# Performance work log

Hardware: AMD Instinct MI355X
Metric: run time of the kernel (lower is better)

The kernel has to match this reference:

```python
import jax, jax.numpy as jnp
import numpy as np

EPS = 1e-5
N_IN, N_OUT = 100000, 400000
C_IN, C = 64, 32
K = 27
M_UP, M_C = 100000, 120000


def _sparse_conv(x, w, in_idx, out_idx, n_out):
    # gather-matmul-scatter over K kernel-offset maps
    g = x[in_idx]                               # [K, M, Cin]
    c = jnp.einsum('kmc,kcd->kmd', g, w)        # [K, M, Cout]
    return jax.ops.segment_sum(c.reshape(-1, c.shape[-1]),
                               out_idx.reshape(-1).astype(jnp.int32),
                               num_segments=n_out)


def _bn(x, gamma, beta):
    # train-mode batch norm over the voxel dimension
    m = jnp.mean(x, axis=0)
    v = jnp.var(x, axis=0)
    return (x - m) * jax.lax.rsqrt(v + EPS) * gamma + beta


def setup_inputs() -> dict:
    key = jax.random.key(0)
    ks = jax.random.split(key, 12)
    inp = {
        'x': jax.random.normal(ks[0], (N_IN, C_IN), jnp.float32),
        'x_skip': jax.random.normal(ks[1], (N_OUT, C), jnp.float32),
        'w_up': jax.random.normal(ks[2], (K, C_IN, C), jnp.float32) * 0.05,
        'b_up': jnp.zeros((C,), jnp.float32),
        'g_up': jnp.ones((C,), jnp.float32),
        'bt_up': jnp.zeros((C,), jnp.float32),
        'w1': jax.random.normal(ks[3], (K, 2 * C, C), jnp.float32) * 0.05,
        'g1': jnp.ones((C,), jnp.float32),
        'bt1': jnp.zeros((C,), jnp.float32),
        'w2': jax.random.normal(ks[4], (K, C, C), jnp.float32) * 0.05,
        'g2': jnp.ones((C,), jnp.float32),
        'bt2': jnp.zeros((C,), jnp.float32),
        'up_in_idx': jax.random.randint(ks[5], (K, M_UP), 0, N_IN, jnp.int32),
        'up_out_idx': jax.random.randint(ks[6], (K, M_UP), 0, N_OUT, jnp.int32),
        'c1_in_idx': jax.random.randint(ks[7], (K, M_C), 0, N_OUT, jnp.int32),
        'c1_out_idx': jax.random.randint(ks[8], (K, M_C), 0, N_OUT, jnp.int32),
        'c2_in_idx': jax.random.randint(ks[9], (K, M_C), 0, N_OUT, jnp.int32),
        'c2_out_idx': jax.random.randint(ks[10], (K, M_C), 0, N_OUT, jnp.int32),
    }
    return inp


def reference(x, x_skip, w_up, b_up, g_up, bt_up, w1, g1, bt1, w2, g2, bt2,
              up_in_idx, up_out_idx, c1_in_idx, c1_out_idx, c2_in_idx, c2_out_idx):
    n_out = x_skip.shape[0]
    # transposed sparse upconv onto the skip grid (+ bias)
    h = _sparse_conv(x, w_up, up_in_idx, up_out_idx, n_out) + b_up
    h = jax.nn.relu(_bn(h, g_up, bt_up))
    # jcat along channel dim
    h = jnp.concatenate([h, x_skip], axis=1)      # [N_out, 2C]
    # conv1 (3x3x3, bias=False) + BN + ReLU
    h = _sparse_conv(h, w1, c1_in_idx, c1_out_idx, n_out)
    h = jax.nn.relu(_bn(h, g1, bt1))
    # conv2 (3x3x3, bias=False) + BN + ReLU
    h = _sparse_conv(h, w2, c2_in_idx, c2_out_idx, n_out)
    h = jax.nn.relu(_bn(h, g2, bt2))
    return h
```

## Files before the change

kernel.cpp:

```cpp
#include <hip/hip_runtime.h>

#define EPS_BN 1e-5f

typedef unsigned int u32;
typedef short short8 __attribute__((ext_vector_type(8)));
typedef float f32x16 __attribute__((ext_vector_type(16)));
typedef _Float16 h4 __attribute__((ext_vector_type(4)));
typedef _Float16 h8f __attribute__((ext_vector_type(8)));

constexpr int N_IN_C  = 100000;
constexpr int N_OUT_C = 400000;
constexpr int KTAPS   = 27;
constexpr int M_UP_C  = 100000;
constexpr int M_C_C   = 120000;

constexpr int WIN     = 256;
constexpr int SH      = 8;
constexpr int NWIN    = (N_OUT_C + WIN - 1) / WIN;
constexpr int NWIN_U  = (N_IN_C  + WIN - 1) / WIN;
constexpr int NBA     = NWIN * KTAPS;
constexpr int NBT     = 3 * NBA;
constexpr int SCHUNK  = 2048;
constexpr int FCH     = 8192;
constexpr int NCHK    = 15;
constexpr int MAXW    = 1600;
constexpr int WSLOTS  = 7;
constexpr int NTILES  = N_OUT_C / 128;
constexpr int HSZ     = 3 * KTAPS * NCHK * NWIN;
constexpr int ENTT    = 27 * (M_UP_C + 2 * M_C_C) + NBT * 31 + 64;

__device__ inline unsigned short f2bf(float f) {
    u32 u = __builtin_bit_cast(u32, f);
    return (unsigned short)((u + 0x7FFFu + ((u >> 16) & 1u)) >> 16);
}

__global__ __launch_bounds__(256) void cvt_kernel(
    const float* __restrict__ s, ushort* __restrict__ d, int n4)
{
    const int i = blockIdx.x * 256 + threadIdx.x;
    if (i >= n4) return;
    const float4 v = reinterpret_cast<const float4*>(s)[i];
    ushort4 o;
    o.x = f2bf(v.x); o.y = f2bf(v.y); o.z = f2bf(v.z); o.w = f2bf(v.w);
    reinterpret_cast<ushort4*>(d)[i] = o;
}

__global__ __launch_bounds__(256) void wpack_kernel(
    const float* __restrict__ wU, const float* __restrict__ w1,
    const float* __restrict__ w2,
    ushort* __restrict__ fU, ushort* __restrict__ f1, ushort* __restrict__ f2)
{
    const int t = blockIdx.x * 256 + threadIdx.x;
    const float* w; ushort* dst; int CIN, NF, local;
    if      (t <  6912) { w = wU; dst = fU; CIN = 64; NF = 4; local = t; }
    else if (t < 13824) { w = w1; dst = f1; CIN = 64; NF = 4; local = t - 6912; }
    else if (t < 17280) { w = w2; dst = f2; CIN = 32; NF = 2; local = t - 13824; }
    else return;
    const int lane = local & 63;
    const int fi   = (local >> 6) % NF;
    const int tap  = local / (64 * NF);
    const int half = lane >> 5, colc = lane & 31;
    ushort* o = dst + ((size_t)(tap * NF + fi) * 64 + lane) * 8;
#pragma unroll
    for (int j = 0; j < 8; ++j) {
        const int k = 16 * fi + 8 * half + j;
        o[j] = f2bf(w[((size_t)tap * CIN + k) * 32 + colc]);
    }
}

__global__ __launch_bounds__(256) void histx_kernel(
    const int* __restrict__ i0, const int* __restrict__ i1,
    const int* __restrict__ i2, u32* __restrict__ h)
{
    const int s = blockIdx.z, k = blockIdx.y, c = blockIdx.x;
    const int M    = (s == 0) ? M_UP_C : M_C_C;
    const int nwin = (s == 0) ? NWIN_U : NWIN;
    const int m0 = c * FCH;
    if (m0 >= M) return;
    const int cnt = min(FCH, M - m0);
    const int* idx = (s == 0) ? i0 : (s == 1) ? i1 : i2;

    __shared__ u32 lh[NWIN];
    for (int w = threadIdx.x; w < nwin; w += 256) lh[w] = 0;
    __syncthreads();
    const int* ink = idx + (size_t)k * M + m0;
    for (int i = threadIdx.x; i < cnt; i += 256)
        atomicAdd(&lh[ink[i] >> SH], 1u);
    __syncthreads();
    u32* hp = h + ((size_t)(s * KTAPS + k) * NCHK + c) * NWIN;
    for (int w = threadIdx.x; w < nwin; w += 256) hp[w] = lh[w];
}

__global__ __launch_bounds__(256) void totals_kernel(
    const u32* __restrict__ h, u32* __restrict__ cnt)
{
    const int s = blockIdx.z, k = blockIdx.y;
    const int w = blockIdx.x * 256 + threadIdx.x;
    if (w >= NWIN) return;
    const u32* hp = h + (size_t)(s * KTAPS + k) * NCHK * NWIN + w;
    u32 t = 0;
#pragma unroll
    for (int c = 0; c < NCHK; ++c) t += hp[(size_t)c * NWIN];
    cnt[(size_t)s * NBA + w * KTAPS + k] = t;
}

__global__ __launch_bounds__(256) void scan_part_kernel(
    const u32* __restrict__ cnt, u32* __restrict__ bsum, int nb)
{
    const int i0 = blockIdx.x * SCHUNK + threadIdx.x * 8;
    u32 s = 0;
#pragma unroll
    for (int j = 0; j < 8; ++j) {
        const int i = i0 + j;
        if (i < nb) s += (cnt[i] + 31u) & ~31u;
    }
    __shared__ u32 ls[256];
    ls[threadIdx.x] = s;
    __syncthreads();
    for (int off = 128; off > 0; off >>= 1) {
        if (threadIdx.x < off) ls[threadIdx.x] += ls[threadIdx.x + off];
        __syncthreads();
    }
    if (threadIdx.x == 0) bsum[blockIdx.x] = ls[0];
}

__global__ __launch_bounds__(1024) void scan_bsum_kernel(
    u32* __restrict__ bsum, int nblk)
{
    __shared__ u32 tmp[1024];
    const int t = threadIdx.x;
    const u32 v = (t < nblk) ? bsum[t] : 0u;
    tmp[t] = v;
    __syncthreads();
    for (int off = 1; off < 1024; off <<= 1) {
        const u32 u = (t >= off) ? tmp[t - off] : 0u;
        __syncthreads();
        tmp[t] += u;
        __syncthreads();
    }
    if (t < nblk) bsum[t] = tmp[t] - v;
}

__global__ __launch_bounds__(256) void scan_emit_kernel(
    const u32* __restrict__ cnt, const u32* __restrict__ bsum,
    u32* __restrict__ starts, int nb)
{
    const int t  = threadIdx.x;
    const int i0 = blockIdx.x * SCHUNK + t * 8;
    u32 vals[8];
    u32 s = 0;
#pragma unroll
    for (int j = 0; j < 8; ++j) {
        const int i = i0 + j;
        u32 c = (i < nb) ? cnt[i] : 0u;
        c = (c + 31u) & ~31u;
        vals[j] = c;
        s += c;
    }
    __shared__ u32 ls[256];
    ls[t] = s;
    __syncthreads();
    for (int off = 1; off < 256; off <<= 1) {
        const u32 u = (t >= off) ? ls[t - off] : 0u;
        __syncthreads();
        ls[t] += u;
        __syncthreads();
    }
    u32 run = bsum[blockIdx.x] + ls[t] - s;
#pragma unroll
    for (int j = 0; j < 8; ++j) {
        const int i = i0 + j;
        if (i < nb) starts[i] = run;
        run += vals[j];
    }
    if (blockIdx.x == gridDim.x - 1 && t == 255) starts[nb] = run;
}

__global__ __launch_bounds__(256) void pbase_kernel(
    const u32* __restrict__ h, const u32* __restrict__ starts,
    u32* __restrict__ pb)
{
    const int s = blockIdx.z, k = blockIdx.y;
    const int w = blockIdx.x * 256 + threadIdx.x;
    if (w >= NWIN) return;
    u32 run = starts[(size_t)s * NBA + w * KTAPS + k];
    const size_t base = (size_t)(s * KTAPS + k) * NCHK * NWIN + w;
#pragma unroll
    for (int c = 0; c < NCHK; ++c) {
        pb[base + (size_t)c * NWIN] = run;
        run += h[base + (size_t)c * NWIN];
    }
}

__global__ __launch_bounds__(256) void fill_kernel(
    const int* __restrict__ in0, const int* __restrict__ out0,
    const int* __restrict__ in1, const int* __restrict__ out1,
    const int* __restrict__ in2, const int* __restrict__ out2,
    const u32* __restrict__ pb, u32* __restrict__ entryA)
{
    __shared__ u32 hist[MAXW];
    __shared__ u32 lofs[MAXW];
    __shared__ u32 gbase[MAXW];
    __shared__ u32 lent[FCH];
    __shared__ u32 psum[256];

    const int s = blockIdx.z;
    const int* in_idx  = (s == 0) ? in0  : (s == 1) ? in1  : in2;
    const int* out_idx = (s == 0) ? out0 : (s == 1) ? out1 : out2;
    const int  M       = (s == 0) ? M_UP_C : M_C_C;
    const int  nwin    = (s == 0) ? NWIN_U : NWIN;

    const int k   = blockIdx.y;
    const int m0  = blockIdx.x * FCH;
    if (m0 >= M) return;
    const int cnt = min(FCH, M - m0);
    const int t   = threadIdx.x;

    const u32* pbk = pb + ((size_t)(s * KTAPS + k) * NCHK + blockIdx.x) * NWIN;

    for (int w = t; w < nwin; w += 256) {
        hist[w]  = 0;
        gbase[w] = pbk[w];
    }
    __syncthreads();

    const int* ink  = in_idx  + (size_t)k * M + m0;
    const int* outk = out_idx + (size_t)k * M + m0;

    for (int i = t; i < cnt; i += 256)
        atomicAdd(&hist[ink[i] >> SH], 1u);
    __syncthreads();

    u32 loc[WSLOTS];
    u32 ssum = 0;
#pragma unroll
    for (int j = 0; j < WSLOTS; ++j) {
        const int w = t * WSLOTS + j;
        const u32 c = (w < nwin) ? hist[w] : 0u;
        loc[j] = ssum;
        ssum += c;
    }
    psum[t] = ssum;
    __syncthreads();
    for (int off = 1; off < 256; off <<= 1) {
        const u32 v = (t >= off) ? psum[t - off] : 0u;
        __syncthreads();
        psum[t] += v;
        __syncthreads();
    }
    const u32 tbase = psum[t] - ssum;
#pragma unroll
    for (int j = 0; j < WSLOTS; ++j) {
        const int w = t * WSLOTS + j;
        if (w < nwin) lofs[w] = tbase + loc[j];
    }
    __syncthreads();

    for (int i = t; i < cnt; i += 256) {
        const int in = ink[i];
        const int o  = outk[i];
        const int w  = in >> SH;
        const u32 pp = atomicAdd(&lofs[w], 1u);
        lent[pp] = ((u32)(in & (WIN - 1)) << 19) | (u32)o;
    }
    __syncthreads();

    for (int w = t; w < nwin; w += 256) {
        const u32 c = hist[w];
        if (!c) continue;
        const u32 lo = lofs[w] - c;
        const u32 gb = gbase[w];
        for (u32 j = 0; j < c; ++j)
            entryA[gb + j] = lent[lo + j];
    }
}

template <int NF, int MODE>
__global__ __launch_bounds__(256) void conv_kernel(
    const void* __restrict__ srcAv, const void* __restrict__ srcBv,
    const ushort* __restrict__ wfrag,
    const u32* __restrict__ entryA, const u32* __restrict__ starts,
    const float* __restrict__ st, const float* __restrict__ g,
    const float* __restrict__ bt, float invn,
    _Float16* __restrict__ accH, int n_src)
{
    constexpr int NCH = NF * 2;
    constexpr int RPL = 8 / NCH;
    __shared__ ushort win[WIN * NF * 16];

    const int w0   = blockIdx.x * WIN;
    const int tid  = threadIdx.x;
    const int lane = tid & 63;
    const int wid  = tid >> 6;
    const int col  = lane & 31;
    const int half = lane >> 5;
    const int ch0  = tid % NCH;

    float sc8[8], bi8[8];
    const bool needbn = (MODE == 2) || (MODE == 1 && ch0 < 4);
    if (MODE != 0 && needbn) {
#pragma unroll
        for (int j = 0; j < 8; ++j) {
            const int c = ch0 * 8 + j;
            const float m   = st[c] * invn;
            const float var = fmaxf(st[32 + c] * invn - m * m, 0.f);
            const float s_  = rsqrtf(var + EPS_BN) * g[c];
            sc8[j] = s_;
            bi8[j] = fmaf(-m, s_, bt[c]);
        }
    }

    for (int i = tid; i < WIN * NCH; i += 256) {
        const int r  = i / NCH;
        const int row = w0 + r;
        short8 v = {0, 0, 0, 0, 0, 0, 0, 0};
        if (row < n_src) {
            if (MODE == 0) {
                const float* sp = (const float*)srcAv + (size_t)row * 64 + ch0 * 8;
#pragma unroll
                for (int j = 0; j < 8; ++j) v[j] = (short)f2bf(sp[j]);
            } else if (MODE == 1) {
                if (ch0 < 4) {
                    const h8f hv = *reinterpret_cast<const h8f*>(
                        (const _Float16*)srcAv + (size_t)row * 32 + ch0 * 8);
#pragma unroll
                    for (int j = 0; j < 8; ++j) {
                        const float y = fmaf(sc8[j], (float)hv[j], bi8[j]);
                        v[j] = (short)f2bf(y > 0.f ? y : 0.f);
                    }
                } else {
                    v = *reinterpret_cast<const short8*>(
                        (const ushort*)srcBv + (size_t)row * 32 + (ch0 - 4) * 8);
                }
            } else {
                const h8f hv = *reinterpret_cast<const h8f*>(
                    (const _Float16*)srcAv + (size_t)row * 32 + ch0 * 8);
#pragma unroll
                for (int j = 0; j < 8; ++j) {
                    const float y = fmaf(sc8[j], (float)hv[j], bi8[j]);
                    v[j] = (short)f2bf(y > 0.f ? y : 0.f);
                }
            }
        }
        const int addr = (r / RPL) * 64 + ((((r % RPL) * NCH + ch0) ^ ((r / RPL) & 7)) * 8);
        *reinterpret_cast<short8*>(&win[addr]) = v;
    }
    __syncthreads();

    const short8* wf8 = reinterpret_cast<const short8*>(wfrag);

    for (int tap = blockIdx.y * 4 + wid; tap < KTAPS; tap += 8) {
        short8 bf[NF];
#pragma unroll
        for (int f = 0; f < NF; ++f) bf[f] = wf8[(tap * NF + f) * 64 + lane];

        const int b  = blockIdx.x * KTAPS + tap;
        const int s0 = (int)starts[b];
        const int s1 = (int)starts[b + 1];

        for (int bb = s0; bb < s1; bb += 32) {
            const u32 e  = entryA[bb + col];
            const int r  = (int)(e >> 19) & (WIN - 1);
            const int ro = (int)(e & 0x7FFFFu);

            short8 af[NF];
#pragma unroll
            for (int f = 0; f < NF; ++f) {
                const int ch   = f * 2 + half;
                const int addr = (r / RPL) * 64 +
                                 ((((r % RPL) * NCH + ch) ^ ((r / RPL) & 7)) * 8);
                af[f] = *reinterpret_cast<const short8*>(&win[addr]);
            }

            f32x16 cacc;
#pragma unroll
            for (int rr = 0; rr < 16; ++rr) cacc[rr] = 0.f;
#pragma unroll
            for (int f = 0; f < NF; ++f)
                cacc = __builtin_amdgcn_mfma_f32_32x32x16_bf16(af[f], bf[f], cacc, 0, 0, 0);

            const bool oddl = lane & 1;
#pragma unroll
            for (int rr = 0; rr < 16; rr += 2) {
                const int pr0  = (rr & 3) + 8 * (rr >> 2) + 4 * half;
                const int pr1  = ((rr + 1) & 3) + 8 * ((rr + 1) >> 2) + 4 * half;
                const int row0 = __shfl(ro, pr0);
                const int row1 = __shfl(ro, pr1);
                const float a  = cacc[rr], bb2 = cacc[rr + 1];
                const float a2 = __shfl_xor(a, 1);
                const float b2 = __shfl_xor(bb2, 1);
                const float lo = oddl ? b2  : a;
                const float hi = oddl ? bb2 : a2;
                const int  row = oddl ? row1 : row0;
                if (row != 0x7FFFF) {
                    const u32 pk = __builtin_bit_cast(u32,
                        __builtin_amdgcn_cvt_pkrtz(lo, hi));
                    void* ap = (char*)accH + ((size_t)row << 6) + ((u32)(col >> 1) << 2);
                    asm volatile("global_atomic_pk_add_f16 %0, %1, off"
                                 :: "v"(ap), "v"(pk) : "memory");
                }
            }
        }
    }
}

__global__ __launch_bounds__(256) void stats_kernel(
    const _Float16* __restrict__ accH, float* __restrict__ stats)
{
    const int tile = blockIdx.x;
    const int tid  = threadIdx.x;
    const int grp  = tid >> 3;
    const int j    = tid & 7;
    float cs[4] = {0.f, 0.f, 0.f, 0.f};
    float cq[4] = {0.f, 0.f, 0.f, 0.f};
    for (int rr = grp; rr < 128; rr += 32) {
        const h4 v = *reinterpret_cast<const h4*>(
            &accH[(size_t)(tile * 128 + rr) * 32 + j * 4]);
#pragma unroll
        for (int jj = 0; jj < 4; ++jj) {
            const float f = (float)v[jj];
            cs[jj] += f;
            cq[jj] = fmaf(f, f, cq[jj]);
        }
    }
    __shared__ float ls[32][33], lq[32][33];
#pragma unroll
    for (int jj = 0; jj < 4; ++jj) {
        ls[grp][j * 4 + jj] = cs[jj];
        lq[grp][j * 4 + jj] = cq[jj];
    }
    __syncthreads();
    if (tid < 32) {
        float ts = 0.f, tq = 0.f;
#pragma unroll
        for (int gg = 0; gg < 32; ++gg) { ts += ls[gg][tid]; tq += lq[gg][tid]; }
        unsafeAtomicAdd(&stats[tid], ts);
        unsafeAtomicAdd(&stats[32 + tid], tq);
    }
}

__global__ __launch_bounds__(256) void bnout_kernel(
    const _Float16* __restrict__ hsrc,
    const float* __restrict__ stats,
    const float* __restrict__ g,
    const float* __restrict__ bt,
    float* __restrict__ dst, int n)
{
    const int i = blockIdx.x * 256 + threadIdx.x;
    if (i >= n * 8) return;
    const h4 v = *reinterpret_cast<const h4*>(&hsrc[(size_t)i * 4]);
    const int c0 = (i & 7) * 4;
    const float invn = 1.f / (float)n;
    float o[4];
#pragma unroll
    for (int j = 0; j < 4; ++j) {
        const int c   = c0 + j;
        const float m   = stats[c] * invn;
        const float var = fmaxf(stats[32 + c] * invn - m * m, 0.f);
        const float s_  = rsqrtf(var + EPS_BN) * g[c];
        float y = ((float)v[j] - m) * s_ + bt[c];
        o[j] = y > 0.f ? y : 0.f;
    }
    float4 w = {o[0], o[1], o[2], o[3]};
    reinterpret_cast<float4*>(dst)[i] = w;
}

extern "C" void kernel_launch(void* const* d_in, const int* in_sizes, int n_in,
                              void* d_out, int out_size, void* d_ws, size_t ws_size,
                              hipStream_t stream)
{
    const float* x      = (const float*)d_in[0];
    const float* x_skip = (const float*)d_in[1];
    const float* w_up   = (const float*)d_in[2];
    const float* g_up   = (const float*)d_in[4];
    const float* bt_up  = (const float*)d_in[5];
    const float* w1     = (const float*)d_in[6];
    const float* g1     = (const float*)d_in[7];
    const float* bt1    = (const float*)d_in[8];
    const float* w2     = (const float*)d_in[9];
    const float* g2     = (const float*)d_in[10];
    const float* bt2    = (const float*)d_in[11];
    const int* up_in    = (const int*)d_in[12];
    const int* up_out   = (const int*)d_in[13];
    const int* c1_in    = (const int*)d_in[14];
    const int* c1_out   = (const int*)d_in[15];
    const int* c2_in    = (const int*)d_in[16];
    const int* c2_out   = (const int*)d_in[17];

    char* p = (char*)d_ws;
    auto alloc = [&](size_t bytes) { char* r = p; p += (bytes + 255) & ~(size_t)255; return r; };
    _Float16* accA   = (_Float16*) alloc((size_t)N_OUT_C * 32 * 2);
    _Float16* accB   = (_Float16*) alloc((size_t)N_OUT_C * 32 * 2);
    ushort*   skip16 = (ushort*)   alloc((size_t)N_OUT_C * 32 * 2);
    ushort*   wfU    = (ushort*)   alloc(27 * 4 * 64 * 8 * 2);
    ushort*   wf1    = (ushort*)   alloc(27 * 4 * 64 * 8 * 2);
    ushort*   wf2    = (ushort*)   alloc(27 * 2 * 64 * 8 * 2);
    float*    stats  = (float*)    alloc(192 * 4);
    u32*      bsum   = (u32*)      alloc(1024 * 4);
    u32*      htab   = (u32*)      alloc((size_t)HSZ * 4);
    u32*      pbase  = (u32*)      alloc((size_t)HSZ * 4);
    u32*      cnt    = (u32*)      alloc((size_t)NBT * 4);
    u32*      starts = (u32*)      alloc((size_t)(NBT + 1) * 4);
    u32*      entryA = (u32*)      alloc((size_t)ENTT * 4);

    float* out = (float*)d_out;
    const dim3 blk(256);
    const float invn = 1.f / (float)N_OUT_C;
    const int nblkS = (NBT + SCHUNK - 1) / SCHUNK;
    const dim3 gChunk(NCHK, KTAPS, 3);
    const dim3 gWinKS((NWIN + 255) / 256, KTAPS, 3);
    const int bn_blocks = (N_OUT_C * 8 + 255) / 256;
    const size_t accBytes = (size_t)N_OUT_C * 32 * 2;

    wpack_kernel<<<(17280 + 255) / 256, blk, 0, stream>>>(w_up, w1, w2, wfU, wf1, wf2);
    cvt_kernel<<<(N_OUT_C * 8 + 255) / 256, blk, 0, stream>>>(x_skip, skip16, N_OUT_C * 8);
    hipMemsetAsync(stats, 0, 192 * sizeof(float), stream);
    hipMemsetAsync(htab, 0, (size_t)HSZ * 4, stream);
    hipMemsetAsync(entryA, 0xFF, (size_t)ENTT * 4, stream);
    histx_kernel<<<gChunk, blk, 0, stream>>>(up_in, c1_in, c2_in, htab);
    totals_kernel<<<gWinKS, blk, 0, stream>>>(htab, cnt);
    scan_part_kernel<<<nblkS, blk, 0, stream>>>(cnt, bsum, NBT);
    scan_bsum_kernel<<<1, 1024, 0, stream>>>(bsum, nblkS);
    scan_emit_kernel<<<nblkS, blk, 0, stream>>>(cnt, bsum, starts, NBT);
    pbase_kernel<<<gWinKS, blk, 0, stream>>>(htab, starts, pbase);
    fill_kernel<<<gChunk, blk, 0, stream>>>(up_in, up_out, c1_in, c1_out,
                                            c2_in, c2_out, pbase, entryA);

    hipMemsetAsync(accA, 0, accBytes, stream);
    conv_kernel<4, 0><<<dim3(NWIN_U, 2), blk, 0, stream>>>(
        x, nullptr, wfU, entryA, starts, stats, g_up, bt_up, invn, accA, N_IN_C);
    stats_kernel<<<NTILES, blk, 0, stream>>>(accA, stats);

    hipMemsetAsync(accB, 0, accBytes, stream);
    conv_kernel<4, 1><<<dim3(NWIN, 2), blk, 0, stream>>>(
        accA, skip16, wf1, entryA, starts + NBA, stats, g_up, bt_up, invn, accB, N_OUT_C);
    stats_kernel<<<NTILES, blk, 0, stream>>>(accB, stats + 64);

    hipMemsetAsync(accA, 0, accBytes, stream);
    conv_kernel<2, 2><<<dim3(NWIN, 2), blk, 0, stream>>>(
        accB, nullptr, wf2, entryA, starts + 2 * NBA, stats + 64, g1, bt1, invn, accA, N_OUT_C);
    stats_kernel<<<NTILES, blk, 0, stream>>>(accA, stats + 128);

    bnout_kernel<<<bn_blocks, blk, 0, stream>>>(accA, stats + 128, g2, bt2, out, N_OUT_C);
}
```

Before: 955.9 us.

## Drop bucket padding, fuse skip conversion and accumulator zeroing into other kernels

Stops rounding each bucket to a multiple of 32 entries and instead masks lanes past the bucket end in the conv loop. This removes the large 0xFF memset of the entry table and shrinks it. The separate x_skip fp32-to-bf16 conversion kernel is dropped, and conv1 now converts skip rows on the fly while staging them. Zeroing of the next accumulator moves into the stats kernel instead of separate memsets. Together these cut several full-size memory passes and launches, at the cost of extra predication and a wider fp32 skip read inside conv1. The stats kernel must fully read each buffer before it is zeroed for reuse.

```diff
diff --git a/kernel.cpp b/kernel.cpp
--- a/kernel.cpp
+++ b/kernel.cpp
@@ -27,22 +27,11 @@
 constexpr int WSLOTS  = 7;
 constexpr int NTILES  = N_OUT_C / 128;
 constexpr int HSZ     = 3 * KTAPS * NCHK * NWIN;
-constexpr int ENTT    = 27 * (M_UP_C + 2 * M_C_C) + NBT * 31 + 64;
+constexpr int ENTT    = 27 * (M_UP_C + 2 * M_C_C);
 
 __device__ inline unsigned short f2bf(float f) {
     u32 u = __builtin_bit_cast(u32, f);
     return (unsigned short)((u + 0x7FFFu + ((u >> 16) & 1u)) >> 16);
-}
-
-__global__ __launch_bounds__(256) void cvt_kernel(
-    const float* __restrict__ s, ushort* __restrict__ d, int n4)
-{
-    const int i = blockIdx.x * 256 + threadIdx.x;
-    if (i >= n4) return;
-    const float4 v = reinterpret_cast<const float4*>(s)[i];
-    ushort4 o;
-    o.x = f2bf(v.x); o.y = f2bf(v.y); o.z = f2bf(v.z); o.w = f2bf(v.w);
-    reinterpret_cast<ushort4*>(d)[i] = o;
 }
 
 __global__ __launch_bounds__(256) void wpack_kernel(
@@ -112,7 +101,7 @@
 #pragma unroll
     for (int j = 0; j < 8; ++j) {
         const int i = i0 + j;
-        if (i < nb) s += (cnt[i] + 31u) & ~31u;
+        if (i < nb) s += cnt[i];
     }
     __shared__ u32 ls[256];
     ls[threadIdx.x] = s;
@@ -152,8 +141,7 @@
 #pragma unroll
     for (int j = 0; j < 8; ++j) {
         const int i = i0 + j;
-        u32 c = (i < nb) ? cnt[i] : 0u;
-        c = (c + 31u) & ~31u;
+        const u32 c = (i < nb) ? cnt[i] : 0u;
         vals[j] = c;
         s += c;
     }
@@ -329,8 +317,9 @@
                         v[j] = (short)f2bf(y > 0.f ? y : 0.f);
                     }
                 } else {
-                    v = *reinterpret_cast<const short8*>(
-                        (const ushort*)srcBv + (size_t)row * 32 + (ch0 - 4) * 8);
+                    const float* sp = (const float*)srcBv + (size_t)row * 32 + (ch0 - 4) * 8;
+#pragma unroll
+                    for (int j = 0; j < 8; ++j) v[j] = (short)f2bf(sp[j]);
                 }
             } else {
                 const h8f hv = *reinterpret_cast<const h8f*>(
@@ -359,9 +348,10 @@
         const int s1 = (int)starts[b + 1];
 
         for (int bb = s0; bb < s1; bb += 32) {
-            const u32 e  = entryA[bb + col];
+            const bool valid = (bb + col < s1);
+            const u32 e  = valid ? entryA[bb + col] : 0u;
             const int r  = (int)(e >> 19) & (WIN - 1);
-            const int ro = (int)(e & 0x7FFFFu);
+            const int ro = valid ? (int)(e & 0x7FFFFu) : 0x7FFFF;
 
             short8 af[NF];
 #pragma unroll
@@ -405,12 +395,20 @@
 }
 
 __global__ __launch_bounds__(256) void stats_kernel(
-    const _Float16* __restrict__ accH, float* __restrict__ stats)
+    const _Float16* __restrict__ accH, float* __restrict__ stats,
+    float4* __restrict__ zdst)
 {
     const int tile = blockIdx.x;
     const int tid  = threadIdx.x;
     const int grp  = tid >> 3;
     const int j    = tid & 7;
+
+    if (zdst) {
+        const float4 z = {0.f, 0.f, 0.f, 0.f};
+        float4* zp = zdst + (size_t)tile * 512;
+        for (int i = tid; i < 512; i += 256) zp[i] = z;
+    }
+
     float cs[4] = {0.f, 0.f, 0.f, 0.f};
     float cq[4] = {0.f, 0.f, 0.f, 0.f};
     for (int rr = grp; rr < 128; rr += 32) {
@@ -491,7 +489,6 @@
     auto alloc = [&](size_t bytes) { char* r = p; p += (bytes + 255) & ~(size_t)255; return r; };
     _Float16* accA   = (_Float16*) alloc((size_t)N_OUT_C * 32 * 2);
     _Float16* accB   = (_Float16*) alloc((size_t)N_OUT_C * 32 * 2);
-    ushort*   skip16 = (ushort*)   alloc((size_t)N_OUT_C * 32 * 2);
     ushort*   wfU    = (ushort*)   alloc(27 * 4 * 64 * 8 * 2);
     ushort*   wf1    = (ushort*)   alloc(27 * 4 * 64 * 8 * 2);
     ushort*   wf2    = (ushort*)   alloc(27 * 2 * 64 * 8 * 2);
@@ -513,10 +510,8 @@
     const size_t accBytes = (size_t)N_OUT_C * 32 * 2;
 
     wpack_kernel<<<(17280 + 255) / 256, blk, 0, stream>>>(w_up, w1, w2, wfU, wf1, wf2);
-    cvt_kernel<<<(N_OUT_C * 8 + 255) / 256, blk, 0, stream>>>(x_skip, skip16, N_OUT_C * 8);
     hipMemsetAsync(stats, 0, 192 * sizeof(float), stream);
     hipMemsetAsync(htab, 0, (size_t)HSZ * 4, stream);
-    hipMemsetAsync(entryA, 0xFF, (size_t)ENTT * 4, stream);
     histx_kernel<<<gChunk, blk, 0, stream>>>(up_in, c1_in, c2_in, htab);
     totals_kernel<<<gWinKS, blk, 0, stream>>>(htab, cnt);
     scan_part_kernel<<<nblkS, blk, 0, stream>>>(cnt, bsum, NBT);
@@ -529,17 +524,15 @@
     hipMemsetAsync(accA, 0, accBytes, stream);
     conv_kernel<4, 0><<<dim3(NWIN_U, 2), blk, 0, stream>>>(
         x, nullptr, wfU, entryA, starts, stats, g_up, bt_up, invn, accA, N_IN_C);
-    stats_kernel<<<NTILES, blk, 0, stream>>>(accA, stats);
-
-    hipMemsetAsync(accB, 0, accBytes, stream);
+    stats_kernel<<<NTILES, blk, 0, stream>>>(accA, stats, (float4*)accB);
+
     conv_kernel<4, 1><<<dim3(NWIN, 2), blk, 0, stream>>>(
-        accA, skip16, wf1, entryA, starts + NBA, stats, g_up, bt_up, invn, accB, N_OUT_C);
-    stats_kernel<<<NTILES, blk, 0, stream>>>(accB, stats + 64);
-
-    hipMemsetAsync(accA, 0, accBytes, stream);
+        accA, x_skip, wf1, entryA, starts + NBA, stats, g_up, bt_up, invn, accB, N_OUT_C);
+    stats_kernel<<<NTILES, blk, 0, stream>>>(accB, stats + 64, (float4*)accA);
+
     conv_kernel<2, 2><<<dim3(NWIN, 2), blk, 0, stream>>>(
         accB, nullptr, wf2, entryA, starts + 2 * NBA, stats + 64, g1, bt1, invn, accA, N_OUT_C);
-    stats_kernel<<<NTILES, blk, 0, stream>>>(accA, stats + 128);
+    stats_kernel<<<NTILES, blk, 0, stream>>>(accA, stats + 128, nullptr);
 
     bnout_kernel<<<bn_blocks, blk, 0, stream>>>(accA, stats + 128, g2, bt2, out, N_OUT_C);
 }
```

Measured after the change: 912.8 us. 1.05x faster.
